# Performance work log

Measured on AMD Instinct MI355X. Metric: run time of the kernel, lower is better.

The kernel has to match this reference:

```python
import jax, jax.numpy as jnp
import numpy as np

B, U, D = 4096, 256, 128  # batch, units (classes), feature dim


def setup_inputs() -> dict:
    key = jax.random.key(0)
    kx, kw, kb = jax.random.split(key, 3)
    # Scale so points lie well inside the unit Poincare ball (c = 1).
    x = jax.random.normal(kx, (B, D), dtype=jnp.float32) * 0.05
    W = jax.random.normal(kw, (U, D), dtype=jnp.float32) * 0.05
    bias = (jax.random.uniform(kb, (U, D), dtype=jnp.float32) * 2.0 - 1.0) * 0.05
    return {"x": x, "W": W, "bias": bias}


def reference(x, W, bias):
    # c = 1 throughout (module hardcodes c = 1.0).
    def sqnorm(t):
        return jnp.sum(t * t, axis=-1, keepdims=True)

    nb2 = sqnorm(bias)                     # [U,1]  ||p_k||^2
    lam = 2.0 / (1.0 - nb2)                # [U,1]  lambda_{p_k}
    # parallel_transport: lambda_x(0)/lambda_x(bias) * W = (1 - ||bias||^2) * W
    a_k = (1.0 - nb2) * W                  # [U,D]
    a_norm = jnp.sqrt(sqnorm(a_k))         # [U,1]

    # mobius_add(-bias, x), broadcast instead of tiling x to [B,U,D]
    u = -bias[None, :, :]                  # [1,U,D]
    v = x[:, None, :]                      # [B,1,D]
    xy = jnp.sum(u * v, axis=-1, keepdims=True)   # [B,U,1]
    nu2 = nb2[None, :, :]                  # [1,U,1]
    nv2 = sqnorm(v)                        # [B,1,1]
    dd = 1.0 + 2.0 * xy + nu2 * nv2
    m = ((1.0 + 2.0 * xy + nv2) * u + (1.0 - nu2) * v) / dd   # [B,U,D]

    num = 2.0 * jnp.sum(m * a_k[None], axis=-1)               # [B,U]
    den = (1.0 - jnp.sum(m * m, axis=-1)) * a_norm[None, :, 0]  # [B,U]
    logits = (lam * a_norm)[None, :, 0] * jnp.arcsinh(num / den)  # [B,U]
    # exp(logits) / sum(exp(logits)) == softmax(logits) (stable form)
    return jax.nn.softmax(logits, axis=-1)
```

## Files before the change

### kernel.cpp

```cpp
#include <hip/hip_runtime.h>
#include <hip/hip_bf16.h>
#include <math.h>

#define BN 4096
#define UN 256
#define DN 128
#define MROW 16
#define BLOCK 1024
#define LSTRIDE 260

typedef __attribute__((ext_vector_type(8))) short short8x;
typedef __attribute__((ext_vector_type(4))) float float4x;


__device__ inline uint pack2bf(float a, float b) {
    __hip_bfloat16 ha = __float2bfloat16(a);
    __hip_bfloat16 hb = __float2bfloat16(b);
    return (uint)(*(ushort*)&ha) | ((uint)(*(ushort*)&hb) << 16);
}

__global__ __launch_bounds__(1024) void prep_wb(
    const float* __restrict__ W, const float* __restrict__ bias,
    ushort* __restrict__ Wp, ushort* __restrict__ Bp, float4* __restrict__ S)
{
    const int u = blockIdx.x * 16 + (threadIdx.x >> 6);
    const int l = threadIdx.x & 63;
    const float2 w2 = ((const float2*)(W    + (size_t)u * DN))[l];
    const float2 b2 = ((const float2*)(bias + (size_t)u * DN))[l];
    float nb2 = b2.x*b2.x + b2.y*b2.y;
    float bw  = b2.x*w2.x + b2.y*w2.y;
    float wn2 = w2.x*w2.x + w2.y*w2.y;
    #pragma unroll
    for (int off = 32; off; off >>= 1) {
        nb2 += __shfl_xor(nb2, off);
        bw  += __shfl_xor(bw , off);
        wn2 += __shfl_xor(wn2, off);
    }
    const int d  = 2 * l;
    const int ks = d >> 5, q = (d & 31) >> 3, j = d & 7;
    const int chunk = ((u >> 4) * 256) + ks * 64 + q * 16 + (u & 15);
    ((uint*)Wp)[chunk * 4 + (j >> 1)] = pack2bf(w2.x, w2.y);
    ((uint*)Bp)[chunk * 4 + (j >> 1)] = pack2bf(b2.x, b2.y);
    if (l == 0) {
        const float one_m  = 1.0f - nb2;
        const float a_norm = fabsf(one_m) * sqrtf(wn2);
        const float scale  = (2.0f / one_m) * a_norm;
        S[u] = make_float4(nb2, bw, a_norm, scale);
    }
}

__global__ __launch_bounds__(BLOCK, 4) void main_kernel(
    const float* __restrict__ x,
    const ushort* __restrict__ Wp, const ushort* __restrict__ Bp,
    const float4* __restrict__ S, float* __restrict__ out)
{
    __shared__ __align__(16) uint XL[MROW * DN / 2];
    __shared__ float nv2_lds[MROW];
    __shared__ float logits[MROW][LSTRIDE];

    const int t    = threadIdx.x;
    const int lane = t & 63;
    const int wave = t >> 6;
    const int m16  = lane & 15;
    const int q    = lane >> 4;
    const int b0   = blockIdx.x * MROW;
    const int u    = wave * 16 + m16;

    const short8x* wc = (const short8x*)Wp + wave * 256 + lane;
    const short8x* bc = (const short8x*)Bp + wave * 256 + lane;
    short8x wf[4], bf[4];
    #pragma unroll
    for (int ks = 0; ks < 4; ++ks) {
        wf[ks] = wc[ks * 64];
        bf[ks] = bc[ks * 64];
    }
    const float4 sc = S[u];

    {
        const int d0 = lane * 2;
        const float2 v = *(const float2*)(x + (size_t)(b0 + wave) * DN + d0);
        float sq = fmaf(v.x, v.x, v.y * v.y);
        #pragma unroll
        for (int off = 32; off; off >>= 1) sq += __shfl_xor(sq, off);
        if (lane == 0) nv2_lds[wave] = sq;
        const int ks = d0 >> 5, qq = (d0 & 31) >> 3, j = d0 & 7;
        XL[(ks * 64 + qq * 16 + wave) * 4 + (j >> 1)] = pack2bf(v.x, v.y);
    }

    __syncthreads();

    const float4 nv4 = ((const float4*)nv2_lds)[q];
    float4x accW = {0.f, 0.f, 0.f, 0.f};
    float4x accB = {0.f, 0.f, 0.f, 0.f};
    #pragma unroll
    for (int ks = 0; ks < 4; ++ks) {
        const short8x af = *(const short8x*)&XL[(ks * 64 + lane) * 4];
        accW = __builtin_amdgcn_mfma_f32_16x16x32_bf16(af, wf[ks], accW, 0, 0, 0);
        accB = __builtin_amdgcn_mfma_f32_16x16x32_bf16(af, bf[ks], accB, 0, 0, 0);
    }

    const float nb2 = sc.x, bw = sc.y, a_norm = sc.z, scale = sc.w;
    const float one_m = 1.0f - nb2;
    #pragma unroll
    for (int rg = 0; rg < 4; ++rg) {
        const float nv2  = ((const float*)&nv4)[rg];
        const float dot1 = accW[rg];
        const float xy   = -accB[rg];
        const float dd   = 1.0f + 2.0f * xy + nb2 * nv2;
        const float inv_dd = __builtin_amdgcn_rcpf(dd);
        const float alpha  = (1.0f + 2.0f * xy + nv2) * inv_dd;
        const float beta   = one_m * inv_dd;
        const float num = 2.0f * one_m * (beta * dot1 - alpha * bw);
        const float mm  = alpha * alpha * nb2 + 2.0f * alpha * beta * xy
                        + beta * beta * nv2;
        const float den = (1.0f - mm) * a_norm;
        const float z   = num * __builtin_amdgcn_rcpf(den);
        const float s   = sqrtf(fmaf(z, z, 1.0f));
        logits[q * 4 + rg][u] = scale * copysignf(__logf(fabsf(z) + s), z);
    }
    __syncthreads();

    {
        const float4 v = *(const float4*)&logits[wave][lane * 4];
        float mx = fmaxf(fmaxf(v.x, v.y), fmaxf(v.z, v.w));
        #pragma unroll
        for (int off = 32; off; off >>= 1) mx = fmaxf(mx, __shfl_xor(mx, off));
        float4 e;
        e.x = __expf(v.x - mx);  e.y = __expf(v.y - mx);
        e.z = __expf(v.z - mx);  e.w = __expf(v.w - mx);
        float s = e.x + e.y + e.z + e.w;
        #pragma unroll
        for (int off = 32; off; off >>= 1) s += __shfl_xor(s, off);
        const float inv = __builtin_amdgcn_rcpf(s);
        e.x *= inv;  e.y *= inv;  e.z *= inv;  e.w *= inv;
        ((float4*)(out + (size_t)(b0 + wave) * UN))[lane] = e;
    }
}

extern "C" void kernel_launch(void* const* d_in, const int* in_sizes, int n_in,
                              void* d_out, int out_size, void* d_ws, size_t ws_size,
                              hipStream_t stream) {
    const float* x    = (const float*)d_in[0];
    const float* W    = (const float*)d_in[1];
    const float* bias = (const float*)d_in[2];
    float* out = (float*)d_out;

    char* ws = (char*)d_ws;
    ushort* Wp = (ushort*)(ws);
    ushort* Bp = (ushort*)(ws + 65536);
    float4* S  = (float4*)(ws + 131072);

    hipLaunchKernelGGL(prep_wb, dim3(UN / 16), dim3(1024), 0, stream, W, bias, Wp, Bp, S);
    hipLaunchKernelGGL(main_kernel, dim3(BN / MROW), dim3(BLOCK), 0, stream,
                       x, Wp, Bp, S, out);
}
```

Measured before the change: 64.35 us.

## Fuse weight/bias prep into main kernel, removing separate prep launch

Removes the prep kernel that packed W and bias to bf16 MFMA layout and computed per-unit norms. Each block now reads fp32 W and bias rows directly, computes the norms with lane-partial sums and cross-lane shuffles, and packs the bf16 fragments in registers. This drops one kernel launch and the dependency between the two kernels. In exchange, every one of the 256 blocks re-reads the full fp32 W and bias (twice the bytes of bf16) and redoes the packing and norm work.

Result: slower. 67.89 us (+5.5%).

```diff
diff --git a/kernel.cpp b/kernel.cpp
--- a/kernel.cpp
+++ b/kernel.cpp
@@ -12,47 +12,15 @@
 typedef __attribute__((ext_vector_type(8))) short short8x;
 typedef __attribute__((ext_vector_type(4))) float float4x;
 
-
 __device__ inline uint pack2bf(float a, float b) {
     __hip_bfloat16 ha = __float2bfloat16(a);
     __hip_bfloat16 hb = __float2bfloat16(b);
     return (uint)(*(ushort*)&ha) | ((uint)(*(ushort*)&hb) << 16);
 }
 
-__global__ __launch_bounds__(1024) void prep_wb(
-    const float* __restrict__ W, const float* __restrict__ bias,
-    ushort* __restrict__ Wp, ushort* __restrict__ Bp, float4* __restrict__ S)
-{
-    const int u = blockIdx.x * 16 + (threadIdx.x >> 6);
-    const int l = threadIdx.x & 63;
-    const float2 w2 = ((const float2*)(W    + (size_t)u * DN))[l];
-    const float2 b2 = ((const float2*)(bias + (size_t)u * DN))[l];
-    float nb2 = b2.x*b2.x + b2.y*b2.y;
-    float bw  = b2.x*w2.x + b2.y*w2.y;
-    float wn2 = w2.x*w2.x + w2.y*w2.y;
-    #pragma unroll
-    for (int off = 32; off; off >>= 1) {
-        nb2 += __shfl_xor(nb2, off);
-        bw  += __shfl_xor(bw , off);
-        wn2 += __shfl_xor(wn2, off);
-    }
-    const int d  = 2 * l;
-    const int ks = d >> 5, q = (d & 31) >> 3, j = d & 7;
-    const int chunk = ((u >> 4) * 256) + ks * 64 + q * 16 + (u & 15);
-    ((uint*)Wp)[chunk * 4 + (j >> 1)] = pack2bf(w2.x, w2.y);
-    ((uint*)Bp)[chunk * 4 + (j >> 1)] = pack2bf(b2.x, b2.y);
-    if (l == 0) {
-        const float one_m  = 1.0f - nb2;
-        const float a_norm = fabsf(one_m) * sqrtf(wn2);
-        const float scale  = (2.0f / one_m) * a_norm;
-        S[u] = make_float4(nb2, bw, a_norm, scale);
-    }
-}
-
-__global__ __launch_bounds__(BLOCK, 4) void main_kernel(
-    const float* __restrict__ x,
-    const ushort* __restrict__ Wp, const ushort* __restrict__ Bp,
-    const float4* __restrict__ S, float* __restrict__ out)
+__global__ __launch_bounds__(BLOCK, 4) void fused_kernel(
+    const float* __restrict__ x, const float* __restrict__ W,
+    const float* __restrict__ bias, float* __restrict__ out)
 {
     __shared__ __align__(16) uint XL[MROW * DN / 2];
     __shared__ float nv2_lds[MROW];
@@ -66,26 +34,55 @@
     const int b0   = blockIdx.x * MROW;
     const int u    = wave * 16 + m16;
 
-    const short8x* wc = (const short8x*)Wp + wave * 256 + lane;
-    const short8x* bc = (const short8x*)Bp + wave * 256 + lane;
+    const int d0x = lane * 2;
+    const float2 xv = *(const float2*)(x + (size_t)(b0 + wave) * DN + d0x);
+
+    const float4* Wrow = (const float4*)(W    + (size_t)u * DN);
+    const float4* Brow = (const float4*)(bias + (size_t)u * DN);
+    float4 wv[8], bv[8];
+    #pragma unroll
+    for (int ks = 0; ks < 4; ++ks) {
+        const int c = ks * 8 + q * 2;
+        wv[2*ks  ] = Wrow[c    ];
+        wv[2*ks+1] = Wrow[c + 1];
+        bv[2*ks  ] = Brow[c    ];
+        bv[2*ks+1] = Brow[c + 1];
+    }
+
+    {
+        float sq = fmaf(xv.x, xv.x, xv.y * xv.y);
+        #pragma unroll
+        for (int off = 32; off; off >>= 1) sq += __shfl_xor(sq, off);
+        if (lane == 0) nv2_lds[wave] = sq;
+        const int ks = d0x >> 5, qq = (d0x & 31) >> 3;
+        XL[(ks * 64 + qq * 16 + wave) * 4 + ((d0x & 7) >> 1)] = pack2bf(xv.x, xv.y);
+    }
+
+    float nb2 = 0.f, bw = 0.f, wn2 = 0.f;
     short8x wf[4], bf[4];
     #pragma unroll
     for (int ks = 0; ks < 4; ++ks) {
-        wf[ks] = wc[ks * 64];
-        bf[ks] = bc[ks * 64];
+        const float* wp = (const float*)&wv[2*ks];
+        const float* bp = (const float*)&bv[2*ks];
+        uint wpk[4], bpk[4];
+        #pragma unroll
+        for (int p = 0; p < 4; ++p) {
+            const float w0 = wp[2*p], w1 = wp[2*p+1];
+            const float c0 = bp[2*p], c1 = bp[2*p+1];
+            wn2 = fmaf(w0, w0, fmaf(w1, w1, wn2));
+            nb2 = fmaf(c0, c0, fmaf(c1, c1, nb2));
+            bw  = fmaf(c0, w0, fmaf(c1, w1, bw));
+            wpk[p] = pack2bf(w0, w1);
+            bpk[p] = pack2bf(c0, c1);
+        }
+        wf[ks] = *(const short8x*)wpk;
+        bf[ks] = *(const short8x*)bpk;
     }
-    const float4 sc = S[u];
-
-    {
-        const int d0 = lane * 2;
-        const float2 v = *(const float2*)(x + (size_t)(b0 + wave) * DN + d0);
-        float sq = fmaf(v.x, v.x, v.y * v.y);
-        #pragma unroll
-        for (int off = 32; off; off >>= 1) sq += __shfl_xor(sq, off);
-        if (lane == 0) nv2_lds[wave] = sq;
-        const int ks = d0 >> 5, qq = (d0 & 31) >> 3, j = d0 & 7;
-        XL[(ks * 64 + qq * 16 + wave) * 4 + (j >> 1)] = pack2bf(v.x, v.y);
-    }
+    nb2 += __shfl_xor(nb2, 16);  bw += __shfl_xor(bw, 16);  wn2 += __shfl_xor(wn2, 16);
+    nb2 += __shfl_xor(nb2, 32);  bw += __shfl_xor(bw, 32);  wn2 += __shfl_xor(wn2, 32);
+    const float one_m  = 1.0f - nb2;
+    const float a_norm = fabsf(one_m) * sqrtf(wn2);
+    const float scale  = (2.0f / one_m) * a_norm;
 
     __syncthreads();
 
@@ -99,8 +96,6 @@
         accB = __builtin_amdgcn_mfma_f32_16x16x32_bf16(af, bf[ks], accB, 0, 0, 0);
     }
 
-    const float nb2 = sc.x, bw = sc.y, a_norm = sc.z, scale = sc.w;
-    const float one_m = 1.0f - nb2;
     #pragma unroll
     for (int rg = 0; rg < 4; ++rg) {
         const float nv2  = ((const float*)&nv4)[rg];
@@ -144,13 +139,8 @@
     const float* W    = (const float*)d_in[1];
     const float* bias = (const float*)d_in[2];
     float* out = (float*)d_out;
+    (void)d_ws; (void)ws_size;
 
-    char* ws = (char*)d_ws;
-    ushort* Wp = (ushort*)(ws);
-    ushort* Bp = (ushort*)(ws + 65536);
-    float4* S  = (float4*)(ws + 131072);
-
-    hipLaunchKernelGGL(prep_wb, dim3(UN / 16), dim3(1024), 0, stream, W, bias, Wp, Bp, S);
-    hipLaunchKernelGGL(main_kernel, dim3(BN / MROW), dim3(BLOCK), 0, stream,
-                       x, Wp, Bp, S, out);
+    hipLaunchKernelGGL(fused_kernel, dim3(BN / MROW), dim3(BLOCK), 0, stream,
+                       x, W, bias, out);
 }
```
